# Performance work log

Hardware: AMD Instinct MI355X
Metric: run time of the kernel (lower is better)

Reference implementation:

```python
import jax, jax.numpy as jnp
import numpy as np

SCORE_THR = 0.05
IOU_THR = 0.5
STD = np.array([0.1, 0.1, 0.2, 0.2], dtype=np.float32)


def _regress_and_clip(reg_pred, anchors, h, w):
    # reg_pred [B,4,A], anchors [A,4] (x1,y1,x2,y2) -> boxes [B,A,4]
    std = jnp.asarray(STD)
    widths = anchors[:, 2] - anchors[:, 0]
    heights = anchors[:, 3] - anchors[:, 1]
    cx = anchors[:, 0] + 0.5 * widths
    cy = anchors[:, 1] + 0.5 * heights
    reg = reg_pred * std[None, :, None]
    dx, dy, dw, dh = reg[:, 0], reg[:, 1], reg[:, 2], reg[:, 3]  # each [B,A]
    pred_cx = cx + dx * widths
    pred_cy = cy + dy * heights
    pred_w = jnp.exp(dw) * widths
    pred_h = jnp.exp(dh) * heights
    x1 = jnp.maximum(pred_cx - 0.5 * pred_w, 0.0)
    y1 = pred_cy - 0.5 * pred_h
    x2 = pred_cx + 0.5 * pred_w
    y2 = pred_cy + 0.5 * pred_h
    # clip_anchors
    x1 = jnp.maximum(x1, 0.0)
    y1 = jnp.maximum(y1, 0.0)
    x2 = jnp.minimum(x2, jnp.float32(w))
    y2 = jnp.minimum(y2, jnp.float32(h))
    return jnp.stack([x1, y1, x2, y2], axis=-1)  # [B,A,4] (= permuted boxes_pred)


def _iou_one_vs_all(box, boxes):
    ix1 = jnp.maximum(box[0], boxes[:, 0])
    iy1 = jnp.maximum(box[1], boxes[:, 1])
    ix2 = jnp.minimum(box[2], boxes[:, 2])
    iy2 = jnp.minimum(box[3], boxes[:, 3])
    inter = jnp.maximum(ix2 - ix1, 0.0) * jnp.maximum(iy2 - iy1, 0.0)
    a0 = (box[2] - box[0]) * (box[3] - box[1])
    a1 = (boxes[:, 2] - boxes[:, 0]) * (boxes[:, 3] - boxes[:, 1])
    return inter / jnp.maximum(a0 + a1 - inter, 1e-9)


def _nms_keep(boxes, scores):
    # Greedy NMS (torchvision semantics): returns bool keep mask over all anchors.
    valid = scores > SCORE_THR
    order = jnp.argsort(jnp.where(valid, -scores, jnp.inf))  # desc by score, invalid last
    b = boxes[order]
    keep0 = valid[order]
    n = boxes.shape[0]
    idx = jnp.arange(n)
    def body(i, keep):
        iou = _iou_one_vs_all(b[i], b)
        sup = keep[i] & (iou > IOU_THR) & (idx > i)
        return keep & (~sup)
    keep_sorted = jax.lax.fori_loop(0, n, body, keep0)
    return jnp.zeros(n, dtype=bool).at[order].set(keep_sorted)


def _keep_mask(boxes, cls_pred):
    # boxes [B,A,4], cls_pred [B,C,A] -> keep [B,C,A]
    per_class = jax.vmap(_nms_keep, in_axes=(None, 0))
    return jax.vmap(per_class, in_axes=(0, 0))(boxes, cls_pred)


def setup_inputs() -> dict:
    key = jax.random.key(0)
    k1, k2, k3, k4 = jax.random.split(key, 4)
    B, C, A, H, W = 2, 80, 1024, 2048, 2048
    image = jax.random.normal(k1, (B, 3, H, W), dtype=jnp.float32)
    cls_pred = jax.random.uniform(k2, (B, C, A), dtype=jnp.float32)  # sigmoid-like scores
    reg_pred = jax.random.normal(k3, (B, 4, A), dtype=jnp.float32)
    kc, ks = jax.random.split(k4)
    cxy = jax.random.uniform(kc, (A, 2), minval=0.0, maxval=float(W), dtype=jnp.float32)
    wh = jax.random.uniform(ks, (A, 2), minval=16.0, maxval=256.0, dtype=jnp.float32)
    anchors = jnp.concatenate([cxy - 0.5 * wh, cxy + 0.5 * wh], axis=1)  # [A,4] x1y1x2y2
    return {"image": image, "cls_pred": cls_pred, "reg_pred": reg_pred, "anchors": anchors}


def reference(image, cls_pred, reg_pred, anchors):
    B, _, H, W = image.shape
    boxes = _regress_and_clip(reg_pred, anchors, H, W)      # [B,A,4]
    keep = _keep_mask(boxes, cls_pred)                      # [B,C,A] bool
    scores_out = jnp.where(keep, cls_pred, 0.0)             # [B,C,A]
    boxes_out = jnp.where(keep[..., None], boxes[:, None, :, :], 0.0)  # [B,C,A,4]
    # Fixed-shape packing of the module's ragged [scores, cls, boxes] output:
    # per (batch, class, anchor): (score, x1, y1, x2, y2), zeros where suppressed.
    return jnp.concatenate([scores_out[..., None], boxes_out], axis=-1)  # [B,C,A,5]
```

## Files before the change

kernel.cpp:

```cpp
#include <hip/hip_runtime.h>
#include <stdint.h>

#define BATCH 2
#define NCLS 80
#define NP (BATCH * NCLS)
#define NA 1024
#define NWORD 16
#define NWBLK 64
#define IMG_W 2048.0f
#define IMG_H 2048.0f

__device__ __forceinline__ unsigned enc_f32(float f) {
  unsigned u = __float_as_uint(f);
  return (u & 0x80000000u) ? ~u : (u | 0x80000000u);
}

__device__ __forceinline__ unsigned long long shflx64(unsigned long long v, int m) {
  int lo = __shfl_xor((int)(unsigned)v, m, 64);
  int hi = __shfl_xor((int)(unsigned)(v >> 32), m, 64);
  return ((unsigned long long)(unsigned)hi << 32) | (unsigned)lo;
}

__device__ __forceinline__ void cas64(unsigned long long& x, unsigned long long& y, bool up) {
  if ((x > y) == up) { unsigned long long t = x; x = y; y = t; }
}

__global__ __launch_bounds__(256) void prep_kernel(
    const float* __restrict__ cls_pred,
    const float* __restrict__ reg_pred,
    const float* __restrict__ anchors,
    unsigned long long* __restrict__ skeyG,
    float4* __restrict__ sboxG,
    int* __restrict__ nvalidG,
    unsigned long long* __restrict__ W)
{
#pragma clang fp contract(off)
  const int tid = threadIdx.x;
  __shared__ __align__(16) unsigned char smem[24832];

  if (blockIdx.x < NP) {
    const int bc = blockIdx.x;
    const int b  = bc / NCLS;
    float4*             obox = (float4*)(smem);
    unsigned long long* skey = (unsigned long long*)(smem + 16384);
    int*                cntS = (int*)(smem + 24576);

    if (tid == 0) *cntS = 0;
    __syncthreads();

    const float* regb = reg_pred + (size_t)b * 4 * NA;
    const float* scb  = cls_pred + (size_t)bc * NA;

    float4 s4 = ((const float4*)scb)[tid];
    float4 x4 = ((const float4*)(regb + 0 * NA))[tid];
    float4 y4 = ((const float4*)(regb + 1 * NA))[tid];
    float4 w4 = ((const float4*)(regb + 2 * NA))[tid];
    float4 h4 = ((const float4*)(regb + 3 * NA))[tid];
    float ss[4]  = {s4.x, s4.y, s4.z, s4.w};
    float dxs[4] = {x4.x, x4.y, x4.z, x4.w};
    float dys[4] = {y4.x, y4.y, y4.z, y4.w};
    float dws[4] = {w4.x, w4.y, w4.z, w4.w};
    float dhs[4] = {h4.x, h4.y, h4.z, h4.w};

    unsigned long long r[4];
    int localcnt = 0;
#pragma unroll
    for (int m = 0; m < 4; ++m) {
      const int a = tid * 4 + m;
      float4 an = ((const float4*)anchors)[a];
      float w  = an.z - an.x;
      float h  = an.w - an.y;
      float cx = an.x + 0.5f * w;
      float cy = an.y + 0.5f * h;
      float dx = dxs[m] * 0.1f;
      float dy = dys[m] * 0.1f;
      float dw = dws[m] * 0.2f;
      float dh = dhs[m] * 0.2f;
      float pcx = cx + dx * w;
      float pcy = cy + dy * h;
      float pw  = expf(dw) * w;
      float ph  = expf(dh) * h;
      float x1 = fmaxf(pcx - 0.5f * pw, 0.0f);
      float y1 = pcy - 0.5f * ph;
      x1 = fmaxf(x1, 0.0f);
      y1 = fmaxf(y1, 0.0f);
      float x2 = fminf(pcx + 0.5f * pw, IMG_W);
      float y2 = fminf(pcy + 0.5f * ph, IMG_H);
      obox[a] = make_float4(x1, y1, x2, y2);

      float s    = ss[m];
      bool valid = (s > 0.05f);
      localcnt  += valid ? 1 : 0;
      float key  = valid ? -s : __int_as_float(0x7f800000);
      r[m] = ((unsigned long long)enc_f32(key) << 32) | (unsigned)a;
    }
    atomicAdd(cntS, localcnt);

#pragma unroll
    for (int kk = 1; kk <= 10; ++kk) {
      const int k = 1 << kk;
#pragma unroll
      for (int jj = kk - 1; jj >= 0; --jj) {
        const int j = 1 << jj;
        if (j >= 256) {
          __syncthreads();
#pragma unroll
          for (int m = 0; m < 4; ++m) skey[tid * 4 + m] = r[m];
          __syncthreads();
#pragma unroll
          for (int m = 0; m < 4; ++m) {
            const int e = tid * 4 + m;
            unsigned long long o = skey[e ^ j];
            const bool up = ((e & k) == 0);
            const bool lo = ((e & j) == 0);
            unsigned long long mn = (r[m] < o) ? r[m] : o;
            unsigned long long mx = (r[m] < o) ? o : r[m];
            r[m] = (lo == up) ? mn : mx;
          }
        } else if (j >= 4) {
          const int d = j >> 2;
          const bool lo = ((tid & d) == 0);
#pragma unroll
          for (int m = 0; m < 4; ++m) {
            const int e = tid * 4 + m;
            const bool up = ((e & k) == 0);
            unsigned long long o = shflx64(r[m], d);
            unsigned long long mn = (r[m] < o) ? r[m] : o;
            unsigned long long mx = (r[m] < o) ? o : r[m];
            r[m] = (lo == up) ? mn : mx;
          }
        } else if (j == 2) {
          const bool up = (((tid * 4) & k) == 0);
          cas64(r[0], r[2], up);
          cas64(r[1], r[3], up);
        } else {
          const bool up01 = (((tid * 4 + 0) & k) == 0);
          const bool up23 = (((tid * 4 + 2) & k) == 0);
          cas64(r[0], r[1], up01);
          cas64(r[2], r[3], up23);
        }
      }
    }

    unsigned long long* pk = skeyG + (size_t)bc * NA;
    float4* pb = sboxG + (size_t)bc * NA;
#pragma unroll
    for (int m = 0; m < 4; ++m) {
      unsigned long long kv = r[m];
      pk[tid * 4 + m] = kv;
      pb[tid * 4 + m] = obox[(int)(unsigned)kv];
    }
    if (tid == 0) nvalidG[bc] = *cntS;

  } else {
    const int wb   = blockIdx.x - NP;
    const int b    = wb >> 5;
    const int sub  = wb & 31;
    const int rblk = sub >> 1;
    const int qh   = sub & 1;
    const int lane = tid & 63;
    const int wq   = tid >> 6;

    float4* sb = (float4*)(smem);

    const float* regb = reg_pred + (size_t)b * 4 * NA;
    {
      float4 x4 = ((const float4*)(regb + 0 * NA))[tid];
      float4 y4 = ((const float4*)(regb + 1 * NA))[tid];
      float4 w4 = ((const float4*)(regb + 2 * NA))[tid];
      float4 h4 = ((const float4*)(regb + 3 * NA))[tid];
      float dxs[4] = {x4.x, x4.y, x4.z, x4.w};
      float dys[4] = {y4.x, y4.y, y4.z, y4.w};
      float dws[4] = {w4.x, w4.y, w4.z, w4.w};
      float dhs[4] = {h4.x, h4.y, h4.z, h4.w};
#pragma unroll
      for (int m = 0; m < 4; ++m) {
        const int a = tid * 4 + m;
        float4 an = ((const float4*)anchors)[a];
        float w  = an.z - an.x;
        float h  = an.w - an.y;
        float cx = an.x + 0.5f * w;
        float cy = an.y + 0.5f * h;
        float dx = dxs[m] * 0.1f;
        float dy = dys[m] * 0.1f;
        float dw = dws[m] * 0.2f;
        float dh = dhs[m] * 0.2f;
        float pcx = cx + dx * w;
        float pcy = cy + dy * h;
        float pw  = expf(dw) * w;
        float ph  = expf(dh) * h;
        float x1 = fmaxf(pcx - 0.5f * pw, 0.0f);
        float y1 = pcy - 0.5f * ph;
        x1 = fmaxf(x1, 0.0f);
        y1 = fmaxf(y1, 0.0f);
        float x2 = fminf(pcx + 0.5f * pw, IMG_W);
        float y2 = fminf(pcy + 0.5f * ph, IMG_H);
        sb[a] = make_float4(x1, y1, x2, y2);
      }
    }
    __syncthreads();

    const int r = rblk * 64 + lane;
    float4 br = sb[r];
    float  ar = (br.z - br.x) * (br.w - br.y);
    unsigned long long* wrow = W + ((size_t)b * NA + r) * NWORD;

#pragma unroll
    for (int k2 = 0; k2 < 2; ++k2) {
      const int kw = qh * 8 + wq * 2 + k2;
      const int jbase = kw * 64;
      unsigned long long bits = 0ull;
#pragma unroll 8
      for (int jj = 0; jj < 64; ++jj) {
        float4 bj = sb[jbase + jj];
        float  aj = (bj.z - bj.x) * (bj.w - bj.y);
        float ix1 = fmaxf(br.x, bj.x);
        float iy1 = fmaxf(br.y, bj.y);
        float ix2 = fminf(br.z, bj.z);
        float iy2 = fminf(br.w, bj.w);
        float inter = fmaxf(ix2 - ix1, 0.0f) * fmaxf(iy2 - iy1, 0.0f);
        float un = fmaxf((ar + aj) - inter, 1e-9f);
        bool sup = ((inter + inter) - un) > un * 5.9604644775390625e-8f;
        bits |= sup ? (1ull << jj) : 0ull;
      }
      wrow[kw] = bits;
    }
  }
}

__global__ __launch_bounds__(256) void scan_kernel(
    const unsigned long long* __restrict__ skeyG,
    const float4* __restrict__ sboxG,
    const unsigned long long* __restrict__ W,
    const int* __restrict__ nvalidG,
    float* __restrict__ out)
{
  const int p    = blockIdx.x;
  const int b    = p / NCLS;
  const int tid  = threadIdx.x;
  const int lane = tid & 63;
  const int wid  = tid >> 6;

  __shared__ unsigned long long rowsL[3][64 * 17];
  __shared__ unsigned long long diagLo[2][64];
  __shared__ unsigned long long diagHi[2][64];
  __shared__ int oL[NA];
  __shared__ unsigned long long KorigL[NWORD];
  __shared__ unsigned long long keptS[NWORD];
  __shared__ __align__(16) float outAll[NA * 5];

  if (tid < NWORD) { KorigL[tid] = 0ull; keptS[tid] = 0ull; }

  const int nv = nvalidG[p];
  const int nchunk = (nv + 63) >> 6;
  const unsigned long long* pk = skeyG + (size_t)p * NA;
  const unsigned long long* Wb = W + (size_t)b * NA * NWORD;

#pragma unroll
  for (int t = 0; t < 4; ++t) {
    int r = t * 256 + tid;
    oL[r] = (int)(unsigned)pk[r];
  }
  __syncthreads();

  if (nchunk > 0) {
    const int half = wid >> 1;
    const int slot = tid & 127;
    const int rsub8 = slot >> 4;
    const int wsubp = slot & 15;
    if (half == 0 || nchunk > 1) {
      const int cbase = half * 64;
      unsigned long long pre0[8];
#pragma unroll
      for (int t = 0; t < 8; ++t) {
        int orow = oL[cbase + t * 8 + rsub8];
        pre0[t] = Wb[(size_t)orow * NWORD + wsubp];
      }
#pragma unroll
      for (int t = 0; t < 8; ++t)
        rowsL[half][(t * 8 + rsub8) * 17 + wsubp] = pre0[t];
    }
  }
  __syncthreads();

  const int rsub = lane >> 4;
  const int wsub = lane & 15;

  unsigned long long pre[16];

  if (nchunk > 0 && wid >= 2) {
    const int sbase = (wid - 2) * 32;
    int om = oL[lane];
    int wsel = om >> 6, bsel = om & 63;
    unsigned long long d = 0ull;
#pragma unroll 16
    for (int s = 0; s < 32; ++s) {
      int si = sbase + s;
      d |= ((rowsL[0][si * 17 + wsel] >> bsel) & 1ull) << si;
    }
    if (wid == 2) diagLo[0][lane] = d; else diagHi[0][lane] = d;
  }
  if (wid == 1 && nchunk > 2) {
#pragma unroll
    for (int t = 0; t < 16; ++t) {
      int orow = oL[2 * 64 + t * 4 + rsub];
      pre[t] = Wb[(size_t)orow * NWORD + wsub];
    }
  }
  __syncthreads();

  for (int c = 0; c < nchunk; ++c) {
    if (wid == 1) {
      if (c + 2 < nchunk) {
        const int nb = (c + 2) % 3;
#pragma unroll
        for (int t = 0; t < 16; ++t)
          rowsL[nb][(t * 4 + rsub) * 17 + wsub] = pre[t];
      }
      if (c + 3 < nchunk) {
#pragma unroll
        for (int t = 0; t < 16; ++t) {
          int orow = oL[(c + 3) * 64 + t * 4 + rsub];
          pre[t] = Wb[(size_t)orow * NWORD + wsub];
        }
      }
    } else if (wid >= 2) {
      if (c + 1 < nchunk) {
        const int nb = (c + 1) % 3;
        const int par = (c + 1) & 1;
        const int sbase = (wid - 2) * 32;
        int om = oL[(c + 1) * 64 + lane];
        int wsel = om >> 6, bsel = om & 63;
        unsigned long long d = 0ull;
#pragma unroll 16
        for (int s = 0; s < 32; ++s) {
          int si = sbase + s;
          d |= ((rowsL[nb][si * 17 + wsel] >> bsel) & 1ull) << si;
        }
        if (wid == 2) diagLo[par][lane] = d; else diagHi[par][lane] = d;
      }
    } else {
      const int cb  = c % 3;
      const int par = c & 1;
      const int sMine = c * 64 + lane;
      const int oMine = oL[sMine];

      unsigned long long pp = 0ull;
      if (c) {
#pragma unroll
        for (int k = 0; k < NWORD; ++k)
          pp |= rowsL[cb][lane * 17 + k] & KorigL[k];
      }

      unsigned long long diag =
          (diagLo[par][lane] | diagHi[par][lane]) & ((1ull << lane) - 1ull);

      unsigned long long valid = __ballot(sMine < nv);
      unsigned long long S     = __ballot(pp != 0ull);
      unsigned long long K  = 0ull;
      unsigned long long Dd = (~valid) | S;
      for (int round = 0; round < 64; ++round) {
        unsigned long long und = ~Dd;
        if (und == 0ull) break;
        bool me_und  = (und >> lane) & 1ull;
        bool blocked = (diag & (K | und)) != 0ull;
        bool isSupp  = (diag & K) != 0ull;
        unsigned long long kb  = __ballot(me_und && !blocked);
        unsigned long long sbm = __ballot(me_und && isSupp);
        K  |= kb;
        Dd |= kb | sbm;
      }
      if (lane == 0) keptS[c] = K;

      if ((K >> lane) & 1ull)
        atomicOr(&KorigL[oMine >> 6], 1ull << (oMine & 63));
    }
    __syncthreads();
  }

  const float4* pb = sboxG + (size_t)p * NA;
#pragma unroll
  for (int t = 0; t < 4; ++t) {
    int r = t * 256 + tid;
    unsigned long long kv = pk[r];
    float4 bx = pb[r];
    int orig = (int)(unsigned)kv;
    bool kp = (keptS[r >> 6] >> (r & 63)) & 1ull;
    float sc = 0.0f;
    float4 ob = make_float4(0.0f, 0.0f, 0.0f, 0.0f);
    if (kp) {
      sc = -__uint_as_float(~(unsigned)(kv >> 32));
      ob = bx;
    }
    float* oa = outAll + (size_t)orig * 5;
    oa[0] = sc; oa[1] = ob.x; oa[2] = ob.y; oa[3] = ob.z; oa[4] = ob.w;
  }
  __syncthreads();

  float4* og = (float4*)(out + (size_t)p * NA * 5);
  const float4* ol = (const float4*)outAll;
  for (int t4 = tid; t4 < (NA * 5) / 4; t4 += 256) og[t4] = ol[t4];
}

__global__ __launch_bounds__(256) void nms_mono_kernel(
    const float* __restrict__ cls_pred,
    const float* __restrict__ reg_pred,
    const float* __restrict__ anchors,
    float* __restrict__ out)
{
#pragma clang fp contract(off)
  const int bc  = blockIdx.x;
  const int b   = bc / NCLS;
  const int tid = threadIdx.x;
  const int BNT = 256, BPT = 4;

  __shared__ __align__(16) unsigned char smem[49152];
  float4*             obox  = (float4*)(smem);
  float4*             sbox  = (float4*)(smem + 16384);
  unsigned long long* skey  = (unsigned long long*)(smem + 32768);
  float*              sarea = (float*)(smem + 40960);
  int*                keepL = (int*)(smem + 45056);

  const float* regb = reg_pred + (size_t)b * 4 * NA;
  const float* scb  = cls_pred + (size_t)bc * NA;
  for (int a = tid; a < NA; a += BNT) {
    float4 an = ((const float4*)anchors)[a];
    float w  = an.z - an.x;
    float h  = an.w - an.y;
    float cx = an.x + 0.5f * w;
    float cy = an.y + 0.5f * h;
    float dx = regb[0 * NA + a] * 0.1f;
    float dy = regb[1 * NA + a] * 0.1f;
    float dw = regb[2 * NA + a] * 0.2f;
    float dh = regb[3 * NA + a] * 0.2f;
    float pcx = cx + dx * w;
    float pcy = cy + dy * h;
    float pw  = expf(dw) * w;
    float ph  = expf(dh) * h;
    float x1 = fmaxf(fmaxf(pcx - 0.5f * pw, 0.0f), 0.0f);
    float y1 = fmaxf(pcy - 0.5f * ph, 0.0f);
    float x2 = fminf(pcx + 0.5f * pw, IMG_W);
    float y2 = fminf(pcy + 0.5f * ph, IMG_H);
    obox[a] = make_float4(x1, y1, x2, y2);
    float s   = scb[a];
    float key = (s > 0.05f) ? -s : __int_as_float(0x7f800000);
    skey[a] = ((unsigned long long)enc_f32(key) << 32) | (unsigned)a;
  }
  __syncthreads();
  for (int k = 2; k <= NA; k <<= 1) {
    for (int j = k >> 1; j > 0; j >>= 1) {
      for (int m = tid; m < NA; m += BNT) {
        int mx = m ^ j;
        if (mx > m) {
          unsigned long long va = skey[m];
          unsigned long long vb = skey[mx];
          bool up = ((m & k) == 0);
          if ((va > vb) == up) { skey[m] = vb; skey[mx] = va; }
        }
      }
      __syncthreads();
    }
  }
  float4 bj[4]; float aj[4]; int kj[4];
#pragma unroll
  for (int m = 0; m < BPT; ++m) {
    int r = tid + m * BNT;
    unsigned long long kv = skey[r];
    int orig = (int)(unsigned)kv;
    float4 bx = obox[orig];
    sbox[r] = bx;
    float ar = (bx.z - bx.x) * (bx.w - bx.y);
    sarea[r] = ar;
    int kp = ((unsigned)(kv >> 32) != 0xFF800000u) ? 1 : 0;
    keepL[r] = kp;
    bj[m] = bx; aj[m] = ar; kj[m] = kp;
  }
  for (int i = 0; i < NA; ++i) {
    __syncthreads();
    if (keepL[i] == 0) continue;
    float4 bi = sbox[i];
    float  ai = sarea[i];
#pragma unroll
    for (int m = 0; m < BPT; ++m) {
      int j = tid + m * BNT;
      if (j > i && kj[m]) {
        float ix1 = fmaxf(bi.x, bj[m].x);
        float iy1 = fmaxf(bi.y, bj[m].y);
        float ix2 = fminf(bi.z, bj[m].z);
        float iy2 = fminf(bi.w, bj[m].w);
        float inter = fmaxf(ix2 - ix1, 0.0f) * fmaxf(iy2 - iy1, 0.0f);
        float un = fmaxf(ai + aj[m] - inter, 1e-9f);
        if (inter / un > 0.5f) { kj[m] = 0; keepL[j] = 0; }
      }
    }
  }
  __syncthreads();
  float4* outbox = obox;
  float*  outsc  = sarea;
#pragma unroll
  for (int m = 0; m < BPT; ++m) {
    int r = tid + m * BNT;
    unsigned long long kv = skey[r];
    int orig = (int)(unsigned)kv;
    float  sc = 0.0f;
    float4 bx = make_float4(0.0f, 0.0f, 0.0f, 0.0f);
    if (kj[m]) {
      sc = -__uint_as_float(~(unsigned)(kv >> 32));
      bx = sbox[r];
    }
    outsc[orig]  = sc;
    outbox[orig] = bx;
  }
  __syncthreads();
  float* ob = out + (size_t)bc * NA * 5;
  for (int a = tid; a < NA; a += BNT) {
    float4 bx = outbox[a];
    float* o = ob + (size_t)a * 5;
    o[0] = outsc[a]; o[1] = bx.x; o[2] = bx.y; o[3] = bx.z; o[4] = bx.w;
  }
}

extern "C" void kernel_launch(void* const* d_in, const int* in_sizes, int n_in,
                              void* d_out, int out_size, void* d_ws, size_t ws_size,
                              hipStream_t stream) {
  const float* cls = (const float*)d_in[1];
  const float* reg = (const float*)d_in[2];
  const float* anc = (const float*)d_in[3];
  float* out = (float*)d_out;

  const size_t off_key = 0;
  const size_t off_box = off_key + (size_t)NP * NA * 8;
  const size_t off_w   = off_box + (size_t)NP * NA * 16;
  const size_t off_nv  = off_w + (size_t)BATCH * NA * NWORD * 8;
  const size_t need    = off_nv + (size_t)NP * sizeof(int);

  if (ws_size < need) {
    nms_mono_kernel<<<dim3(NP), dim3(256), 0, stream>>>(cls, reg, anc, out);
    return;
  }

  char* ws = (char*)d_ws;
  unsigned long long* skeyG = (unsigned long long*)(ws + off_key);
  float4*             sboxG = (float4*)(ws + off_box);
  unsigned long long* Wm    = (unsigned long long*)(ws + off_w);
  int*                nvG   = (int*)(ws + off_nv);

  prep_kernel<<<dim3(NP + NWBLK), dim3(256), 0, stream>>>(
      cls, reg, anc, skeyG, sboxG, nvG, Wm);
  scan_kernel<<<dim3(NP), dim3(256), 0, stream>>>(skeyG, sboxG, Wm, nvG, out);
}
```

Baseline: 149.8 us.

## Fuse per-class sort into scan kernel and split IoU matrix into own kernel

Moves the per-class box regression and bitonic sort from the prep kernel into the scan kernel, so sorted keys, sorted boxes and valid counts no longer round-trip through global workspace. The IoU bitmask build becomes a standalone kernel with twice as many blocks, each computing one 64-bit word per thread instead of two. In exchange the scan kernel now holds the sort and its larger shared-memory footprint on its critical path, and box regression is recomputed per class.

```diff
diff --git a/kernel.cpp b/kernel.cpp
--- a/kernel.cpp
+++ b/kernel.cpp
@@ -6,7 +6,7 @@
 #define NP (BATCH * NCLS)
 #define NA 1024
 #define NWORD 16
-#define NWBLK 64
+#define NWBLK 128
 #define IMG_W 2048.0f
 #define IMG_H 2048.0f
 
@@ -25,45 +25,33 @@
   if ((x > y) == up) { unsigned long long t = x; x = y; y = t; }
 }
 
-__global__ __launch_bounds__(256) void prep_kernel(
-    const float* __restrict__ cls_pred,
+__global__ __launch_bounds__(256) void wmat_kernel(
     const float* __restrict__ reg_pred,
     const float* __restrict__ anchors,
-    unsigned long long* __restrict__ skeyG,
-    float4* __restrict__ sboxG,
-    int* __restrict__ nvalidG,
     unsigned long long* __restrict__ W)
 {
 #pragma clang fp contract(off)
-  const int tid = threadIdx.x;
-  __shared__ __align__(16) unsigned char smem[24832];
-
-  if (blockIdx.x < NP) {
-    const int bc = blockIdx.x;
-    const int b  = bc / NCLS;
-    float4*             obox = (float4*)(smem);
-    unsigned long long* skey = (unsigned long long*)(smem + 16384);
-    int*                cntS = (int*)(smem + 24576);
-
-    if (tid == 0) *cntS = 0;
-    __syncthreads();
-
-    const float* regb = reg_pred + (size_t)b * 4 * NA;
-    const float* scb  = cls_pred + (size_t)bc * NA;
-
-    float4 s4 = ((const float4*)scb)[tid];
+  const int tid  = threadIdx.x;
+  const int wb   = blockIdx.x;
+  const int b    = wb >> 6;
+  const int sub  = wb & 63;
+  const int rblk = sub >> 2;
+  const int qq   = sub & 3;
+  const int lane = tid & 63;
+  const int wq   = tid >> 6;
+
+  __shared__ __align__(16) float4 sb[NA];
+
+  const float* regb = reg_pred + (size_t)b * 4 * NA;
+  {
     float4 x4 = ((const float4*)(regb + 0 * NA))[tid];
     float4 y4 = ((const float4*)(regb + 1 * NA))[tid];
     float4 w4 = ((const float4*)(regb + 2 * NA))[tid];
     float4 h4 = ((const float4*)(regb + 3 * NA))[tid];
-    float ss[4]  = {s4.x, s4.y, s4.z, s4.w};
     float dxs[4] = {x4.x, x4.y, x4.z, x4.w};
     float dys[4] = {y4.x, y4.y, y4.z, y4.w};
     float dws[4] = {w4.x, w4.y, w4.z, w4.w};
     float dhs[4] = {h4.x, h4.y, h4.z, h4.w};
-
-    unsigned long long r[4];
-    int localcnt = 0;
 #pragma unroll
     for (int m = 0; m < 4; ++m) {
       const int a = tid * 4 + m;
@@ -86,182 +74,167 @@
       y1 = fmaxf(y1, 0.0f);
       float x2 = fminf(pcx + 0.5f * pw, IMG_W);
       float y2 = fminf(pcy + 0.5f * ph, IMG_H);
-      obox[a] = make_float4(x1, y1, x2, y2);
-
-      float s    = ss[m];
-      bool valid = (s > 0.05f);
-      localcnt  += valid ? 1 : 0;
-      float key  = valid ? -s : __int_as_float(0x7f800000);
-      r[m] = ((unsigned long long)enc_f32(key) << 32) | (unsigned)a;
-    }
-    atomicAdd(cntS, localcnt);
-
-#pragma unroll
-    for (int kk = 1; kk <= 10; ++kk) {
-      const int k = 1 << kk;
-#pragma unroll
-      for (int jj = kk - 1; jj >= 0; --jj) {
-        const int j = 1 << jj;
-        if (j >= 256) {
-          __syncthreads();
-#pragma unroll
-          for (int m = 0; m < 4; ++m) skey[tid * 4 + m] = r[m];
-          __syncthreads();
-#pragma unroll
-          for (int m = 0; m < 4; ++m) {
-            const int e = tid * 4 + m;
-            unsigned long long o = skey[e ^ j];
-            const bool up = ((e & k) == 0);
-            const bool lo = ((e & j) == 0);
-            unsigned long long mn = (r[m] < o) ? r[m] : o;
-            unsigned long long mx = (r[m] < o) ? o : r[m];
-            r[m] = (lo == up) ? mn : mx;
-          }
-        } else if (j >= 4) {
-          const int d = j >> 2;
-          const bool lo = ((tid & d) == 0);
-#pragma unroll
-          for (int m = 0; m < 4; ++m) {
-            const int e = tid * 4 + m;
-            const bool up = ((e & k) == 0);
-            unsigned long long o = shflx64(r[m], d);
-            unsigned long long mn = (r[m] < o) ? r[m] : o;
-            unsigned long long mx = (r[m] < o) ? o : r[m];
-            r[m] = (lo == up) ? mn : mx;
-          }
-        } else if (j == 2) {
-          const bool up = (((tid * 4) & k) == 0);
-          cas64(r[0], r[2], up);
-          cas64(r[1], r[3], up);
-        } else {
-          const bool up01 = (((tid * 4 + 0) & k) == 0);
-          const bool up23 = (((tid * 4 + 2) & k) == 0);
-          cas64(r[0], r[1], up01);
-          cas64(r[2], r[3], up23);
-        }
-      }
-    }
-
-    unsigned long long* pk = skeyG + (size_t)bc * NA;
-    float4* pb = sboxG + (size_t)bc * NA;
-#pragma unroll
-    for (int m = 0; m < 4; ++m) {
-      unsigned long long kv = r[m];
-      pk[tid * 4 + m] = kv;
-      pb[tid * 4 + m] = obox[(int)(unsigned)kv];
-    }
-    if (tid == 0) nvalidG[bc] = *cntS;
-
-  } else {
-    const int wb   = blockIdx.x - NP;
-    const int b    = wb >> 5;
-    const int sub  = wb & 31;
-    const int rblk = sub >> 1;
-    const int qh   = sub & 1;
-    const int lane = tid & 63;
-    const int wq   = tid >> 6;
-
-    float4* sb = (float4*)(smem);
-
-    const float* regb = reg_pred + (size_t)b * 4 * NA;
-    {
-      float4 x4 = ((const float4*)(regb + 0 * NA))[tid];
-      float4 y4 = ((const float4*)(regb + 1 * NA))[tid];
-      float4 w4 = ((const float4*)(regb + 2 * NA))[tid];
-      float4 h4 = ((const float4*)(regb + 3 * NA))[tid];
-      float dxs[4] = {x4.x, x4.y, x4.z, x4.w};
-      float dys[4] = {y4.x, y4.y, y4.z, y4.w};
-      float dws[4] = {w4.x, w4.y, w4.z, w4.w};
-      float dhs[4] = {h4.x, h4.y, h4.z, h4.w};
-#pragma unroll
-      for (int m = 0; m < 4; ++m) {
-        const int a = tid * 4 + m;
-        float4 an = ((const float4*)anchors)[a];
-        float w  = an.z - an.x;
-        float h  = an.w - an.y;
-        float cx = an.x + 0.5f * w;
-        float cy = an.y + 0.5f * h;
-        float dx = dxs[m] * 0.1f;
-        float dy = dys[m] * 0.1f;
-        float dw = dws[m] * 0.2f;
-        float dh = dhs[m] * 0.2f;
-        float pcx = cx + dx * w;
-        float pcy = cy + dy * h;
-        float pw  = expf(dw) * w;
-        float ph  = expf(dh) * h;
-        float x1 = fmaxf(pcx - 0.5f * pw, 0.0f);
-        float y1 = pcy - 0.5f * ph;
-        x1 = fmaxf(x1, 0.0f);
-        y1 = fmaxf(y1, 0.0f);
-        float x2 = fminf(pcx + 0.5f * pw, IMG_W);
-        float y2 = fminf(pcy + 0.5f * ph, IMG_H);
-        sb[a] = make_float4(x1, y1, x2, y2);
-      }
-    }
-    __syncthreads();
-
-    const int r = rblk * 64 + lane;
-    float4 br = sb[r];
-    float  ar = (br.z - br.x) * (br.w - br.y);
-    unsigned long long* wrow = W + ((size_t)b * NA + r) * NWORD;
-
-#pragma unroll
-    for (int k2 = 0; k2 < 2; ++k2) {
-      const int kw = qh * 8 + wq * 2 + k2;
-      const int jbase = kw * 64;
-      unsigned long long bits = 0ull;
+      sb[a] = make_float4(x1, y1, x2, y2);
+    }
+  }
+  __syncthreads();
+
+  const int r = rblk * 64 + lane;
+  float4 br = sb[r];
+  float  ar = (br.z - br.x) * (br.w - br.y);
+
+  const int kw = qq * 4 + wq;
+  const int jbase = kw * 64;
+  unsigned long long bits = 0ull;
 #pragma unroll 8
-      for (int jj = 0; jj < 64; ++jj) {
-        float4 bj = sb[jbase + jj];
-        float  aj = (bj.z - bj.x) * (bj.w - bj.y);
-        float ix1 = fmaxf(br.x, bj.x);
-        float iy1 = fmaxf(br.y, bj.y);
-        float ix2 = fminf(br.z, bj.z);
-        float iy2 = fminf(br.w, bj.w);
-        float inter = fmaxf(ix2 - ix1, 0.0f) * fmaxf(iy2 - iy1, 0.0f);
-        float un = fmaxf((ar + aj) - inter, 1e-9f);
-        bool sup = ((inter + inter) - un) > un * 5.9604644775390625e-8f;
-        bits |= sup ? (1ull << jj) : 0ull;
-      }
-      wrow[kw] = bits;
-    }
-  }
-}
-
-__global__ __launch_bounds__(256) void scan_kernel(
-    const unsigned long long* __restrict__ skeyG,
-    const float4* __restrict__ sboxG,
+  for (int jj = 0; jj < 64; ++jj) {
+    float4 bj = sb[jbase + jj];
+    float  aj = (bj.z - bj.x) * (bj.w - bj.y);
+    float ix1 = fmaxf(br.x, bj.x);
+    float iy1 = fmaxf(br.y, bj.y);
+    float ix2 = fminf(br.z, bj.z);
+    float iy2 = fminf(br.w, bj.w);
+    float inter = fmaxf(ix2 - ix1, 0.0f) * fmaxf(iy2 - iy1, 0.0f);
+    float un = fmaxf((ar + aj) - inter, 1e-9f);
+    bool sup = ((inter + inter) - un) > un * 5.9604644775390625e-8f;
+    bits |= sup ? (1ull << jj) : 0ull;
+  }
+  W[((size_t)b * NA + r) * NWORD + kw] = bits;
+}
+
+__global__ __launch_bounds__(256) void sortscan_kernel(
+    const float* __restrict__ cls_pred,
+    const float* __restrict__ reg_pred,
+    const float* __restrict__ anchors,
     const unsigned long long* __restrict__ W,
-    const int* __restrict__ nvalidG,
     float* __restrict__ out)
 {
-  const int p    = blockIdx.x;
-  const int b    = p / NCLS;
-  const int tid  = threadIdx.x;
+#pragma clang fp contract(off)
+  const int tid = threadIdx.x;
+  __shared__ __align__(16) unsigned char smem[48912];
+  float4*             obox  = (float4*)(smem);
+  unsigned long long* skey  = (unsigned long long*)(smem + 16384);
+  int*                oL    = (int*)(smem + 16384);
+  unsigned long long* rowsL = (unsigned long long*)(smem + 20480);
+  unsigned long long* diagLo= (unsigned long long*)(smem + 46592);
+  unsigned long long* diagHi= (unsigned long long*)(smem + 47616);
+  unsigned long long* KorigL= (unsigned long long*)(smem + 48640);
+  unsigned long long* keptS = (unsigned long long*)(smem + 48768);
+  int*                cntS  = (int*)(smem + 48896);
+  float*              outAll= (float*)(smem + 16384);
+
+  const int bc = blockIdx.x;
+  const int b  = bc / NCLS;
+
+  if (tid == 0) *cntS = 0;
+  __syncthreads();
+
+  const float* regb = reg_pred + (size_t)b * 4 * NA;
+  const float* scb  = cls_pred + (size_t)bc * NA;
+
+  float4 s4 = ((const float4*)scb)[tid];
+  float4 x4 = ((const float4*)(regb + 0 * NA))[tid];
+  float4 y4 = ((const float4*)(regb + 1 * NA))[tid];
+  float4 w4 = ((const float4*)(regb + 2 * NA))[tid];
+  float4 h4 = ((const float4*)(regb + 3 * NA))[tid];
+  float ss[4]  = {s4.x, s4.y, s4.z, s4.w};
+  float dxs[4] = {x4.x, x4.y, x4.z, x4.w};
+  float dys[4] = {y4.x, y4.y, y4.z, y4.w};
+  float dws[4] = {w4.x, w4.y, w4.z, w4.w};
+  float dhs[4] = {h4.x, h4.y, h4.z, h4.w};
+
+  unsigned long long r[4];
+  int localcnt = 0;
+#pragma unroll
+  for (int m = 0; m < 4; ++m) {
+    const int a = tid * 4 + m;
+    float4 an = ((const float4*)anchors)[a];
+    float w  = an.z - an.x;
+    float h  = an.w - an.y;
+    float cx = an.x + 0.5f * w;
+    float cy = an.y + 0.5f * h;
+    float dx = dxs[m] * 0.1f;
+    float dy = dys[m] * 0.1f;
+    float dw = dws[m] * 0.2f;
+    float dh = dhs[m] * 0.2f;
+    float pcx = cx + dx * w;
+    float pcy = cy + dy * h;
+    float pw  = expf(dw) * w;
+    float ph  = expf(dh) * h;
+    float x1 = fmaxf(pcx - 0.5f * pw, 0.0f);
+    float y1 = pcy - 0.5f * ph;
+    x1 = fmaxf(x1, 0.0f);
+    y1 = fmaxf(y1, 0.0f);
+    float x2 = fminf(pcx + 0.5f * pw, IMG_W);
+    float y2 = fminf(pcy + 0.5f * ph, IMG_H);
+    obox[a] = make_float4(x1, y1, x2, y2);
+
+    float s    = ss[m];
+    bool valid = (s > 0.05f);
+    localcnt  += valid ? 1 : 0;
+    float key  = valid ? -s : __int_as_float(0x7f800000);
+    r[m] = ((unsigned long long)enc_f32(key) << 32) | (unsigned)a;
+  }
+  atomicAdd(cntS, localcnt);
+
+#pragma unroll
+  for (int kk = 1; kk <= 10; ++kk) {
+    const int k = 1 << kk;
+#pragma unroll
+    for (int jj = kk - 1; jj >= 0; --jj) {
+      const int j = 1 << jj;
+      if (j >= 256) {
+        __syncthreads();
+#pragma unroll
+        for (int m = 0; m < 4; ++m) skey[tid * 4 + m] = r[m];
+        __syncthreads();
+#pragma unroll
+        for (int m = 0; m < 4; ++m) {
+          const int e = tid * 4 + m;
+          unsigned long long o = skey[e ^ j];
+          const bool up = ((e & k) == 0);
+          const bool lo = ((e & j) == 0);
+          unsigned long long mn = (r[m] < o) ? r[m] : o;
+          unsigned long long mx = (r[m] < o) ? o : r[m];
+          r[m] = (lo == up) ? mn : mx;
+        }
+      } else if (j >= 4) {
+        const int d = j >> 2;
+        const bool lo = ((tid & d) == 0);
+#pragma unroll
+        for (int m = 0; m < 4; ++m) {
+          const int e = tid * 4 + m;
+          const bool up = ((e & k) == 0);
+          unsigned long long o = shflx64(r[m], d);
+          unsigned long long mn = (r[m] < o) ? r[m] : o;
+          unsigned long long mx = (r[m] < o) ? o : r[m];
+          r[m] = (lo == up) ? mn : mx;
+        }
+      } else if (j == 2) {
+        const bool up = (((tid * 4) & k) == 0);
+        cas64(r[0], r[2], up);
+        cas64(r[1], r[3], up);
+      } else {
+        const bool up01 = (((tid * 4 + 0) & k) == 0);
+        const bool up23 = (((tid * 4 + 2) & k) == 0);
+        cas64(r[0], r[1], up01);
+        cas64(r[2], r[3], up23);
+      }
+    }
+  }
+
   const int lane = tid & 63;
   const int wid  = tid >> 6;
 
-  __shared__ unsigned long long rowsL[3][64 * 17];
-  __shared__ unsigned long long diagLo[2][64];
-  __shared__ unsigned long long diagHi[2][64];
-  __shared__ int oL[NA];
-  __shared__ unsigned long long KorigL[NWORD];
-  __shared__ unsigned long long keptS[NWORD];
-  __shared__ __align__(16) float outAll[NA * 5];
-
+  __syncthreads();
+#pragma unroll
+  for (int m = 0; m < 4; ++m) oL[tid * 4 + m] = (int)(unsigned)r[m];
   if (tid < NWORD) { KorigL[tid] = 0ull; keptS[tid] = 0ull; }
-
-  const int nv = nvalidG[p];
+  __syncthreads();
+
+  const int nv = *cntS;
   const int nchunk = (nv + 63) >> 6;
-  const unsigned long long* pk = skeyG + (size_t)p * NA;
   const unsigned long long* Wb = W + (size_t)b * NA * NWORD;
-
-#pragma unroll
-  for (int t = 0; t < 4; ++t) {
-    int r = t * 256 + tid;
-    oL[r] = (int)(unsigned)pk[r];
-  }
-  __syncthreads();
 
   if (nchunk > 0) {
     const int half = wid >> 1;
@@ -278,7 +251,7 @@
       }
 #pragma unroll
       for (int t = 0; t < 8; ++t)
-        rowsL[half][(t * 8 + rsub8) * 17 + wsubp] = pre0[t];
+        rowsL[(size_t)half * 1088 + (t * 8 + rsub8) * 17 + wsubp] = pre0[t];
     }
   }
   __syncthreads();
@@ -296,9 +269,9 @@
 #pragma unroll 16
     for (int s = 0; s < 32; ++s) {
       int si = sbase + s;
-      d |= ((rowsL[0][si * 17 + wsel] >> bsel) & 1ull) << si;
-    }
-    if (wid == 2) diagLo[0][lane] = d; else diagHi[0][lane] = d;
+      d |= ((rowsL[si * 17 + wsel] >> bsel) & 1ull) << si;
+    }
+    if (wid == 2) diagLo[lane] = d; else diagHi[lane] = d;
   }
   if (wid == 1 && nchunk > 2) {
 #pragma unroll
@@ -315,7 +288,7 @@
         const int nb = (c + 2) % 3;
 #pragma unroll
         for (int t = 0; t < 16; ++t)
-          rowsL[nb][(t * 4 + rsub) * 17 + wsub] = pre[t];
+          rowsL[(size_t)nb * 1088 + (t * 4 + rsub) * 17 + wsub] = pre[t];
       }
       if (c + 3 < nchunk) {
 #pragma unroll
@@ -335,9 +308,9 @@
 #pragma unroll 16
         for (int s = 0; s < 32; ++s) {
           int si = sbase + s;
-          d |= ((rowsL[nb][si * 17 + wsel] >> bsel) & 1ull) << si;
+          d |= ((rowsL[(size_t)nb * 1088 + si * 17 + wsel] >> bsel) & 1ull) << si;
         }
-        if (wid == 2) diagLo[par][lane] = d; else diagHi[par][lane] = d;
+        if (wid == 2) diagLo[par * 64 + lane] = d; else diagHi[par * 64 + lane] = d;
       }
     } else {
       const int cb  = c % 3;
@@ -349,11 +322,11 @@
       if (c) {
 #pragma unroll
         for (int k = 0; k < NWORD; ++k)
-          pp |= rowsL[cb][lane * 17 + k] & KorigL[k];
+          pp |= rowsL[(size_t)cb * 1088 + lane * 17 + k] & KorigL[k];
       }
 
       unsigned long long diag =
-          (diagLo[par][lane] | diagHi[par][lane]) & ((1ull << lane) - 1ull);
+          (diagLo[par * 64 + lane] | diagHi[par * 64 + lane]) & ((1ull << lane) - 1ull);
 
       unsigned long long valid = __ballot(sMine < nv);
       unsigned long long S     = __ballot(pp != 0ull);
@@ -378,26 +351,24 @@
     __syncthreads();
   }
 
-  const float4* pb = sboxG + (size_t)p * NA;
-#pragma unroll
-  for (int t = 0; t < 4; ++t) {
-    int r = t * 256 + tid;
-    unsigned long long kv = pk[r];
-    float4 bx = pb[r];
+#pragma unroll
+  for (int m = 0; m < 4; ++m) {
+    const int e = tid * 4 + m;
+    unsigned long long kv = r[m];
     int orig = (int)(unsigned)kv;
-    bool kp = (keptS[r >> 6] >> (r & 63)) & 1ull;
+    bool kp = (keptS[e >> 6] >> (e & 63)) & 1ull;
     float sc = 0.0f;
     float4 ob = make_float4(0.0f, 0.0f, 0.0f, 0.0f);
     if (kp) {
       sc = -__uint_as_float(~(unsigned)(kv >> 32));
-      ob = bx;
+      ob = obox[orig];
     }
     float* oa = outAll + (size_t)orig * 5;
     oa[0] = sc; oa[1] = ob.x; oa[2] = ob.y; oa[3] = ob.z; oa[4] = ob.w;
   }
   __syncthreads();
 
-  float4* og = (float4*)(out + (size_t)p * NA * 5);
+  float4* og = (float4*)(out + (size_t)bc * NA * 5);
   const float4* ol = (const float4*)outAll;
   for (int t4 = tid; t4 < (NA * 5) / 4; t4 += 256) og[t4] = ol[t4];
 }
@@ -528,24 +499,15 @@
   const float* anc = (const float*)d_in[3];
   float* out = (float*)d_out;
 
-  const size_t off_key = 0;
-  const size_t off_box = off_key + (size_t)NP * NA * 8;
-  const size_t off_w   = off_box + (size_t)NP * NA * 16;
-  const size_t off_nv  = off_w + (size_t)BATCH * NA * NWORD * 8;
-  const size_t need    = off_nv + (size_t)NP * sizeof(int);
+  const size_t need = (size_t)BATCH * NA * NWORD * 8;
 
   if (ws_size < need) {
     nms_mono_kernel<<<dim3(NP), dim3(256), 0, stream>>>(cls, reg, anc, out);
     return;
   }
 
-  char* ws = (char*)d_ws;
-  unsigned long long* skeyG = (unsigned long long*)(ws + off_key);
-  float4*             sboxG = (float4*)(ws + off_box);
-  unsigned long long* Wm    = (unsigned long long*)(ws + off_w);
-  int*                nvG   = (int*)(ws + off_nv);
-
-  prep_kernel<<<dim3(NP + NWBLK), dim3(256), 0, stream>>>(
-      cls, reg, anc, skeyG, sboxG, nvG, Wm);
-  scan_kernel<<<dim3(NP), dim3(256), 0, stream>>>(skeyG, sboxG, Wm, nvG, out);
-}
+  unsigned long long* Wm = (unsigned long long*)d_ws;
+
+  wmat_kernel<<<dim3(NWBLK), dim3(256), 0, stream>>>(reg, anc, Wm);
+  sortscan_kernel<<<dim3(NP), dim3(256), 0, stream>>>(cls, reg, anc, Wm, out);
+}
```

Result: slower. 153.2 us (+2.2%).
